# Kernel optimization log

Measured on AMD Instinct MI355X. Metric: run time of the kernel, lower is better.

The kernel has to match this reference:

```python
import jax, jax.numpy as jnp
import numpy as np

B, D, K = 8192, 256, 3
ALPHA, LAMBDA_NEG, GAMMA_SEMI = 0.7, 0.7, 0.7


def setup_inputs() -> dict:
    key = jax.random.key(0)
    k1, k2, k3 = jax.random.split(key, 3)
    text_embeddings = jax.random.normal(k1, (B, D), dtype=jnp.float32)
    image_embeddings = jax.random.normal(k2, (B, D), dtype=jnp.float32)
    # resolved pseudo-GT indices; -1 marks 'id not found in batch'
    semi_positive_indices = jax.random.randint(k3, (B, K), -1, B).astype(jnp.int32)
    return {
        "text_embeddings": text_embeddings,
        "image_embeddings": image_embeddings,
        "semi_positive_indices": semi_positive_indices,
    }


def _l2_normalize(x, eps=1e-12):
    n = jnp.sqrt(jnp.sum(x * x, axis=1, keepdims=True))
    return x / jnp.maximum(n, eps)


def reference(text_embeddings, image_embeddings, semi_positive_indices):
    t = _l2_normalize(text_embeddings)
    v = _l2_normalize(image_embeddings)
    sim = t @ v.T  # [B, B]
    b = sim.shape[0]

    rows = jnp.arange(b, dtype=semi_positive_indices.dtype)[:, None]  # [B,1]
    idx = semi_positive_indices  # [B,K]
    valid = (idx >= 0) & (idx != rows)  # exclude missing ids and the diagonal
    safe_idx = jnp.clip(idx, 0, b - 1)
    rows_b = jnp.broadcast_to(rows, idx.shape)
    semi_mask = jnp.zeros((b, b), dtype=bool).at[rows_b, safe_idx].max(valid)

    eye = jnp.eye(b, dtype=bool)
    diag = jnp.diagonal(sim)
    l_pos = jnp.sum((diag - 1.0) ** 2)

    semi_term = jnp.where(semi_mask, jnp.maximum(ALPHA - sim, 0.0), 0.0)
    l_semi_pos = jnp.sum(semi_term ** 2)

    neg_mask = ~(eye | semi_mask)
    neg_term = jnp.where(neg_mask, jnp.maximum(sim, 0.0), 0.0)
    l_neg = jnp.sum(neg_term ** 2)

    return l_pos + LAMBDA_NEG * l_neg + GAMMA_SEMI * l_semi_pos
```

## Files before the change

### kernel.cpp

```cpp
#include <hip/hip_runtime.h>

#define BDIM 8192
#define DDIM 256
#define NSLOTS 512

typedef __bf16 bf16x8 __attribute__((ext_vector_type(8)));
typedef float f32x4 __attribute__((ext_vector_type(4)));
typedef unsigned short u16x4 __attribute__((ext_vector_type(4)));

#define MEMF() asm volatile("" ::: "memory")
#define BARR()                       \
  do {                               \
    MEMF();                          \
    __builtin_amdgcn_s_barrier();    \
    MEMF();                          \
  } while (0)
#define VMW(n) asm volatile("s_waitcnt vmcnt(" #n ")" ::: "memory")

__device__ inline unsigned short f2bf(float f) {
  unsigned u = __float_as_uint(f);
  u += 0x7FFFu + ((u >> 16) & 1u);
  return (unsigned short)(u >> 16);
}
__device__ inline float bf2f(unsigned short h) {
  return __uint_as_float(((unsigned)h) << 16);
}

__device__ inline void gload_lds16(const void* g, void* l) {
  __builtin_amdgcn_global_load_lds(
      (const __attribute__((address_space(1))) void*)g,
      (__attribute__((address_space(3))) void*)l, 16, 0, 0);
}

__global__ __launch_bounds__(256) void norm_convert_kernel(
    const float* __restrict__ t, const float* __restrict__ v,
    unsigned short* __restrict__ tn, unsigned short* __restrict__ vn,
    float* __restrict__ slots) {
  int wid = threadIdx.x >> 6, lane = threadIdx.x & 63;
  if (blockIdx.x == 0) {
    slots[threadIdx.x] = 0.0f;
    slots[threadIdx.x + 256] = 0.0f;
  }
  int row = blockIdx.x * 4 + wid;
  const float* src;
  unsigned short* dst;
  if (row < BDIM) {
    src = t + (size_t)row * DDIM;
    dst = tn + (size_t)row * DDIM;
  } else {
    int r = row - BDIM;
    src = v + (size_t)r * DDIM;
    dst = vn + (size_t)r * DDIM;
  }
  float4 x = reinterpret_cast<const float4*>(src)[lane];
  float ss = x.x * x.x + x.y * x.y + x.z * x.z + x.w * x.w;
  #pragma unroll
  for (int off = 1; off < 64; off <<= 1) ss += __shfl_xor(ss, off, 64);
  float sc = 1.0f / fmaxf(sqrtf(ss), 1e-12f);
  u16x4 w;
  w[0] = f2bf(x.x * sc); w[1] = f2bf(x.y * sc);
  w[2] = f2bf(x.z * sc); w[3] = f2bf(x.w * sc);
  reinterpret_cast<u16x4*>(dst)[lane] = w;
}

__global__ __launch_bounds__(512) void loss_kernel(
    const unsigned short* __restrict__ tn,
    const unsigned short* __restrict__ vn, float* __restrict__ slots) {
  __shared__ unsigned short Asb[2][16384];
  __shared__ unsigned short Bsb[2][16384];
  __shared__ float rbuf[8];

  const int tid = threadIdx.x;
  const int lane = tid & 63;
  const int wid = tid >> 6;
  const int l15 = lane & 15;
  const int l4 = lane >> 4;
  const int wm = wid >> 2;
  const int wn = wid & 3;

  const int flat = blockIdx.x;
  const int xcd = flat & 7;
  const int s = flat >> 3;
  const int r = s >> 5;
  const int p = s & 31;
  const int rowp = (xcd >> 2) * 16 + r * 4 + (p >> 3);
  const int colp = (xcd & 3) * 8 + (p & 7);
  const int rowBase = rowp * 256;
  const int colBase = colp * 256;

  const int sg = (tid & 7) ^ ((tid >> 3) & 7);
  const unsigned short* gAsrc =
      tn + (size_t)(rowBase + (tid >> 3)) * DDIM + sg * 8;
  const unsigned short* gBsrc =
      vn + (size_t)(colBase + (tid >> 3)) * DDIM + sg * 8;
  const int ldsStage = wid * 512;

  auto stA = [&](int ob, int rg, int kt) {
    gload_lds16(gAsrc + (size_t)rg * 64 * DDIM + kt * 64,
                &Asb[ob][rg * 4096 + ldsStage]);
  };
  auto stB = [&](int ob, int rg, int kt) {
    gload_lds16(gBsrc + (size_t)rg * 64 * DDIM + kt * 64,
                &Bsb[ob][rg * 4096 + ldsStage]);
  };

  f32x4 acc[8][4];
  #pragma unroll
  for (int i = 0; i < 8; ++i)
    #pragma unroll
    for (int j = 0; j < 4; ++j) acc[i][j] = (f32x4)(0.0f);

  bf16x8 af[4][2], bv0[2][2], bv1[2][2];

  auto readA = [&](int cur, int mh) {
    #pragma unroll
    for (int mm = 0; mm < 4; ++mm) {
      const int row = wm * 128 + (mh * 4 + mm) * 16 + l15;
      #pragma unroll
      for (int kk = 0; kk < 2; ++kk) {
        const int gg = (kk * 4 + l4) ^ (l15 & 7);
        af[mm][kk] =
            *reinterpret_cast<const bf16x8*>(&Asb[cur][row * 64 + gg * 8]);
      }
    }
  };
  auto readB = [&](int cur, int nh, bf16x8 (&bv)[2][2]) {
    #pragma unroll
    for (int nn = 0; nn < 2; ++nn) {
      const int row = wn * 64 + (nh * 2 + nn) * 16 + l15;
      #pragma unroll
      for (int kk = 0; kk < 2; ++kk) {
        const int gg = (kk * 4 + l4) ^ (l15 & 7);
        bv[nn][kk] =
            *reinterpret_cast<const bf16x8*>(&Bsb[cur][row * 64 + gg * 8]);
      }
    }
  };
  auto mfmaQ = [&](int mh, int nh, bf16x8 (&bv)[2][2]) {
    __builtin_amdgcn_s_setprio(1);
    #pragma unroll
    for (int mm = 0; mm < 4; ++mm)
      #pragma unroll
      for (int nn = 0; nn < 2; ++nn)
        #pragma unroll
        for (int kk = 0; kk < 2; ++kk)
          acc[mh * 4 + mm][nh * 2 + nn] =
              __builtin_amdgcn_mfma_f32_16x16x32_bf16(
                  af[mm][kk], bv[nn][kk], acc[mh * 4 + mm][nh * 2 + nn], 0, 0,
                  0);
    __builtin_amdgcn_s_setprio(0);
  };

  stB(0, 0, 0); stB(0, 1, 0); stB(0, 2, 0); stB(0, 3, 0);
  stA(0, 0, 0); stA(0, 1, 0); stA(0, 2, 0); stA(0, 3, 0);
  VMW(0);
  BARR();

  #pragma unroll
  for (int t = 0; t < 4; ++t) {
    const int cur = t & 1, ob = cur ^ 1, kt = t + 1;
    if (t < 3) {
      stB(ob, 0, kt); stB(ob, 1, kt); stB(ob, 2, kt); stB(ob, 3, kt);
      stA(ob, 0, kt); stA(ob, 1, kt); stA(ob, 2, kt); stA(ob, 3, kt);
    }
    readA(cur, 0);
    readB(cur, 0, bv0);
    readB(cur, 1, bv1);
    mfmaQ(0, 0, bv0);
    mfmaQ(0, 1, bv1);
    readA(cur, 1);
    mfmaQ(1, 1, bv1);
    mfmaQ(1, 0, bv0);
    if (t < 3) {
      VMW(0);
      BARR();
    }
  }

  float lsum = 0.0f;
  #pragma unroll
  for (int m = 0; m < 8; ++m)
    #pragma unroll
    for (int n = 0; n < 4; ++n)
      #pragma unroll
      for (int r2 = 0; r2 < 4; ++r2) {
        float u = fmaxf(acc[m][n][r2], 0.0f);
        lsum = fmaf(u, u, lsum);
      }
  lsum *= 0.7f;
  #pragma unroll
  for (int off = 1; off < 64; off <<= 1) lsum += __shfl_xor(lsum, off, 64);
  if (lane == 0) rbuf[wid] = lsum;
  __syncthreads();
  if (tid == 0) {
    float sacc = 0.0f;
    #pragma unroll
    for (int w = 0; w < 8; ++w) sacc += rbuf[w];
    atomicAdd(&slots[flat & (NSLOTS - 1)], sacc);
  }
}

__global__ __launch_bounds__(256) void corr_kernel(
    const unsigned short* __restrict__ tn,
    const unsigned short* __restrict__ vn, const int* __restrict__ sidx,
    float* __restrict__ slots) {
  int wid = threadIdx.x >> 6, lane = threadIdx.x & 63;
  int i = blockIdx.x * 4 + wid;

  u16x4 ta = reinterpret_cast<const u16x4*>(tn + (size_t)i * DDIM)[lane];
  float t0 = bf2f(ta[0]), t1 = bf2f(ta[1]), t2 = bf2f(ta[2]), t3 = bf2f(ta[3]);

  int j0 = sidx[(size_t)i * 3 + 0];
  int j1 = sidx[(size_t)i * 3 + 1];
  int j2 = sidx[(size_t)i * 3 + 2];
  bool v0 = (j0 >= 0) & (j0 < BDIM) & (j0 != i);
  bool v1 = (j1 >= 0) & (j1 < BDIM) & (j1 != i) & !(v0 & (j1 == j0));
  bool v2 = (j2 >= 0) & (j2 < BDIM) & (j2 != i) & !(v0 & (j2 == j0)) &
            !(v1 & (j2 == j1));

  float corr = 0.0f;
  {
    u16x4 va = reinterpret_cast<const u16x4*>(vn + (size_t)i * DDIM)[lane];
    float d = t0 * bf2f(va[0]) + t1 * bf2f(va[1]) + t2 * bf2f(va[2]) +
              t3 * bf2f(va[3]);
    #pragma unroll
    for (int off = 1; off < 64; off <<= 1) d += __shfl_xor(d, off, 64);
    float u = fmaxf(d, 0.0f);
    corr += (d - 1.0f) * (d - 1.0f) - 0.7f * u * u;
  }
  int jj[3] = {j0, j1, j2};
  bool vv[3] = {v0, v1, v2};
  #pragma unroll
  for (int k = 0; k < 3; ++k) {
    int j = vv[k] ? jj[k] : i;
    u16x4 va = reinterpret_cast<const u16x4*>(vn + (size_t)j * DDIM)[lane];
    float d = t0 * bf2f(va[0]) + t1 * bf2f(va[1]) + t2 * bf2f(va[2]) +
              t3 * bf2f(va[3]);
    #pragma unroll
    for (int off = 1; off < 64; off <<= 1) d += __shfl_xor(d, off, 64);
    if (vv[k]) {
      float up = fmaxf(0.7f - d, 0.0f);
      float un = fmaxf(d, 0.0f);
      corr += 0.7f * (up * up - un * un);
    }
  }
  if (lane == 0) atomicAdd(&slots[i & (NSLOTS - 1)], corr);
}

__global__ __launch_bounds__(256) void reduce_kernel(
    const float* __restrict__ slots, float* __restrict__ out) {
  __shared__ float rb[4];
  int tid = threadIdx.x;
  float s = slots[tid] + slots[tid + 256];
  #pragma unroll
  for (int off = 1; off < 64; off <<= 1) s += __shfl_xor(s, off, 64);
  if ((tid & 63) == 0) rb[tid >> 6] = s;
  __syncthreads();
  if (tid == 0) out[0] = rb[0] + rb[1] + rb[2] + rb[3];
}

extern "C" void kernel_launch(void* const* d_in, const int* in_sizes, int n_in,
                              void* d_out, int out_size, void* d_ws,
                              size_t ws_size, hipStream_t stream) {
  const float* t = (const float*)d_in[0];
  const float* v = (const float*)d_in[1];
  const int* sidx = (const int*)d_in[2];
  float* out = (float*)d_out;
  float* slots = (float*)d_ws;
  unsigned short* tn = (unsigned short*)((char*)d_ws + 4096);
  unsigned short* vn = tn + (size_t)BDIM * DDIM;

  norm_convert_kernel<<<4096, 256, 0, stream>>>(t, v, tn, vn, slots);
  loss_kernel<<<1024, 512, 0, stream>>>(tn, vn, slots);
  corr_kernel<<<2048, 256, 0, stream>>>(tn, vn, sidx, slots);
  reduce_kernel<<<1, 256, 0, stream>>>(slots, out);
}
```

Before: 56.35 us.

## Use 4 waves per block with 128x128 per-wave tiles in loss GEMM

The loss kernel drops from 8 waves to 4 per 256x256 block tile, so each wave now computes a 128x128 sub-tile (8x8 MFMA accumulators) instead of 128x64. Each thread issues twice as many global-to-LDS loads, and the interleaved read and MFMA schedule with setprio is replaced by loading all fragments and then running the MFMAs. The aim is more register-level reuse of A and B fragments and fewer LDS reads per MFMA. The cost is much higher register pressure (256 accumulator floats per lane), less latency hiding from having fewer waves, and the loss of the previous read/compute interleaving.

```diff
diff --git a/kernel.cpp b/kernel.cpp
--- a/kernel.cpp
+++ b/kernel.cpp
@@ -63,20 +63,20 @@
   reinterpret_cast<u16x4*>(dst)[lane] = w;
 }
 
-__global__ __launch_bounds__(512) void loss_kernel(
+__global__ __launch_bounds__(256, 1) void loss_kernel(
     const unsigned short* __restrict__ tn,
     const unsigned short* __restrict__ vn, float* __restrict__ slots) {
   __shared__ unsigned short Asb[2][16384];
   __shared__ unsigned short Bsb[2][16384];
-  __shared__ float rbuf[8];
+  __shared__ float rbuf[4];
 
   const int tid = threadIdx.x;
   const int lane = tid & 63;
   const int wid = tid >> 6;
   const int l15 = lane & 15;
   const int l4 = lane >> 4;
-  const int wm = wid >> 2;
-  const int wn = wid & 3;
+  const int wm = wid >> 1;
+  const int wn = wid & 1;
 
   const int flat = blockIdx.x;
   const int xcd = flat & 7;
@@ -93,29 +93,47 @@
       tn + (size_t)(rowBase + (tid >> 3)) * DDIM + sg * 8;
   const unsigned short* gBsrc =
       vn + (size_t)(colBase + (tid >> 3)) * DDIM + sg * 8;
-  const int ldsStage = wid * 512;
+  const int ldsW = wid * 512;
 
   auto stA = [&](int ob, int rg, int kt) {
-    gload_lds16(gAsrc + (size_t)rg * 64 * DDIM + kt * 64,
-                &Asb[ob][rg * 4096 + ldsStage]);
+    #pragma unroll
+    for (int h = 0; h < 2; ++h)
+      gload_lds16(gAsrc + (size_t)(rg * 64 + h * 32) * DDIM + kt * 64,
+                  &Asb[ob][rg * 4096 + h * 2048 + ldsW]);
   };
   auto stB = [&](int ob, int rg, int kt) {
-    gload_lds16(gBsrc + (size_t)rg * 64 * DDIM + kt * 64,
-                &Bsb[ob][rg * 4096 + ldsStage]);
+    #pragma unroll
+    for (int h = 0; h < 2; ++h)
+      gload_lds16(gBsrc + (size_t)(rg * 64 + h * 32) * DDIM + kt * 64,
+                  &Bsb[ob][rg * 4096 + h * 2048 + ldsW]);
   };
 
-  f32x4 acc[8][4];
+  f32x4 acc[8][8];
   #pragma unroll
   for (int i = 0; i < 8; ++i)
     #pragma unroll
-    for (int j = 0; j < 4; ++j) acc[i][j] = (f32x4)(0.0f);
-
-  bf16x8 af[4][2], bv0[2][2], bv1[2][2];
-
-  auto readA = [&](int cur, int mh) {
-    #pragma unroll
-    for (int mm = 0; mm < 4; ++mm) {
-      const int row = wm * 128 + (mh * 4 + mm) * 16 + l15;
+    for (int j = 0; j < 8; ++j) acc[i][j] = (f32x4)(0.0f);
+
+  #pragma unroll
+  for (int rg = 0; rg < 4; ++rg) stB(0, rg, 0);
+  #pragma unroll
+  for (int rg = 0; rg < 4; ++rg) stA(0, rg, 0);
+  VMW(0);
+  BARR();
+
+  #pragma unroll
+  for (int t = 0; t < 4; ++t) {
+    const int cur = t & 1, ob = cur ^ 1, kt = t + 1;
+    if (t < 3) {
+      #pragma unroll
+      for (int rg = 0; rg < 4; ++rg) stB(ob, rg, kt);
+      #pragma unroll
+      for (int rg = 0; rg < 4; ++rg) stA(ob, rg, kt);
+    }
+    bf16x8 af[8][2], bv[8][2];
+    #pragma unroll
+    for (int mm = 0; mm < 8; ++mm) {
+      const int row = wm * 128 + mm * 16 + l15;
       #pragma unroll
       for (int kk = 0; kk < 2; ++kk) {
         const int gg = (kk * 4 + l4) ^ (l15 & 7);
@@ -123,11 +141,9 @@
             *reinterpret_cast<const bf16x8*>(&Asb[cur][row * 64 + gg * 8]);
       }
     }
-  };
-  auto readB = [&](int cur, int nh, bf16x8 (&bv)[2][2]) {
-    #pragma unroll
-    for (int nn = 0; nn < 2; ++nn) {
-      const int row = wn * 64 + (nh * 2 + nn) * 16 + l15;
+    #pragma unroll
+    for (int nn = 0; nn < 8; ++nn) {
+      const int row = wn * 128 + nn * 16 + l15;
       #pragma unroll
       for (int kk = 0; kk < 2; ++kk) {
         const int gg = (kk * 4 + l4) ^ (l15 & 7);
@@ -135,42 +151,14 @@
             *reinterpret_cast<const bf16x8*>(&Bsb[cur][row * 64 + gg * 8]);
       }
     }
-  };
-  auto mfmaQ = [&](int mh, int nh, bf16x8 (&bv)[2][2]) {
-    __builtin_amdgcn_s_setprio(1);
-    #pragma unroll
-    for (int mm = 0; mm < 4; ++mm)
-      #pragma unroll
-      for (int nn = 0; nn < 2; ++nn)
+    #pragma unroll
+    for (int kk = 0; kk < 2; ++kk)
+      #pragma unroll
+      for (int mm = 0; mm < 8; ++mm)
         #pragma unroll
-        for (int kk = 0; kk < 2; ++kk)
-          acc[mh * 4 + mm][nh * 2 + nn] =
-              __builtin_amdgcn_mfma_f32_16x16x32_bf16(
-                  af[mm][kk], bv[nn][kk], acc[mh * 4 + mm][nh * 2 + nn], 0, 0,
-                  0);
-    __builtin_amdgcn_s_setprio(0);
-  };
-
-  stB(0, 0, 0); stB(0, 1, 0); stB(0, 2, 0); stB(0, 3, 0);
-  stA(0, 0, 0); stA(0, 1, 0); stA(0, 2, 0); stA(0, 3, 0);
-  VMW(0);
-  BARR();
-
-  #pragma unroll
-  for (int t = 0; t < 4; ++t) {
-    const int cur = t & 1, ob = cur ^ 1, kt = t + 1;
-    if (t < 3) {
-      stB(ob, 0, kt); stB(ob, 1, kt); stB(ob, 2, kt); stB(ob, 3, kt);
-      stA(ob, 0, kt); stA(ob, 1, kt); stA(ob, 2, kt); stA(ob, 3, kt);
-    }
-    readA(cur, 0);
-    readB(cur, 0, bv0);
-    readB(cur, 1, bv1);
-    mfmaQ(0, 0, bv0);
-    mfmaQ(0, 1, bv1);
-    readA(cur, 1);
-    mfmaQ(1, 1, bv1);
-    mfmaQ(1, 0, bv0);
+        for (int nn = 0; nn < 8; ++nn)
+          acc[mm][nn] = __builtin_amdgcn_mfma_f32_16x16x32_bf16(
+              af[mm][kk], bv[nn][kk], acc[mm][nn], 0, 0, 0);
     if (t < 3) {
       VMW(0);
       BARR();
@@ -181,7 +169,7 @@
   #pragma unroll
   for (int m = 0; m < 8; ++m)
     #pragma unroll
-    for (int n = 0; n < 4; ++n)
+    for (int n = 0; n < 8; ++n)
       #pragma unroll
       for (int r2 = 0; r2 < 4; ++r2) {
         float u = fmaxf(acc[m][n][r2], 0.0f);
@@ -193,10 +181,8 @@
   if (lane == 0) rbuf[wid] = lsum;
   __syncthreads();
   if (tid == 0) {
-    float sacc = 0.0f;
-    #pragma unroll
-    for (int w = 0; w < 8; ++w) sacc += rbuf[w];
-    atomicAdd(&slots[flat & (NSLOTS - 1)], sacc);
+    atomicAdd(&slots[flat & (NSLOTS - 1)],
+              rbuf[0] + rbuf[1] + rbuf[2] + rbuf[3]);
   }
 }
 
@@ -271,7 +257,7 @@
   unsigned short* vn = tn + (size_t)BDIM * DDIM;
 
   norm_convert_kernel<<<4096, 256, 0, stream>>>(t, v, tn, vn, slots);
-  loss_kernel<<<1024, 512, 0, stream>>>(tn, vn, slots);
+  loss_kernel<<<1024, 256, 0, stream>>>(tn, vn, slots);
   corr_kernel<<<2048, 256, 0, stream>>>(tn, vn, sidx, slots);
   reduce_kernel<<<1, 256, 0, stream>>>(slots, out);
 }
```

New measurement: 66.70 us. 1.18x slower.

## Load A fragments directly from global memory and fold final reduction into corr kernel

Applied to the files above, without the earlier changes.

The loss GEMM no longer stages the A (text) tile through LDS. Each wave reads its A fragments straight from global memory into registers, which halves LDS usage and removes the A global-to-LDS copies. The separate reduce kernel is dropped: the last corr block, found with an atomic counter, performs the final slot reduction, saving one kernel launch. The trade-off is uncoalesced, latency-exposed global loads for A that are not prefetched ahead of the MFMAs, plus extra fences and a counter atomic.

```diff
diff --git a/kernel.cpp b/kernel.cpp
--- a/kernel.cpp
+++ b/kernel.cpp
@@ -35,11 +35,12 @@
 __global__ __launch_bounds__(256) void norm_convert_kernel(
     const float* __restrict__ t, const float* __restrict__ v,
     unsigned short* __restrict__ tn, unsigned short* __restrict__ vn,
-    float* __restrict__ slots) {
+    float* __restrict__ slots, unsigned* __restrict__ cnt) {
   int wid = threadIdx.x >> 6, lane = threadIdx.x & 63;
   if (blockIdx.x == 0) {
     slots[threadIdx.x] = 0.0f;
     slots[threadIdx.x + 256] = 0.0f;
+    if (threadIdx.x == 0) cnt[0] = 0u;
   }
   int row = blockIdx.x * 4 + wid;
   const float* src;
@@ -66,7 +67,6 @@
 __global__ __launch_bounds__(512) void loss_kernel(
     const unsigned short* __restrict__ tn,
     const unsigned short* __restrict__ vn, float* __restrict__ slots) {
-  __shared__ unsigned short Asb[2][16384];
   __shared__ unsigned short Bsb[2][16384];
   __shared__ float rbuf[8];
 
@@ -89,21 +89,18 @@
   const int colBase = colp * 256;
 
   const int sg = (tid & 7) ^ ((tid >> 3) & 7);
-  const unsigned short* gAsrc =
-      tn + (size_t)(rowBase + (tid >> 3)) * DDIM + sg * 8;
   const unsigned short* gBsrc =
       vn + (size_t)(colBase + (tid >> 3)) * DDIM + sg * 8;
   const int ldsStage = wid * 512;
 
-  auto stA = [&](int ob, int rg, int kt) {
-    gload_lds16(gAsrc + (size_t)rg * 64 * DDIM + kt * 64,
-                &Asb[ob][rg * 4096 + ldsStage]);
-  };
   auto stB = [&](int ob, int rg, int kt) {
     gload_lds16(gBsrc + (size_t)rg * 64 * DDIM + kt * 64,
                 &Bsb[ob][rg * 4096 + ldsStage]);
   };
 
+  const unsigned short* pA =
+      tn + (size_t)(rowBase + wm * 128 + l15) * DDIM + l4 * 8;
+
   f32x4 acc[8][4];
   #pragma unroll
   for (int i = 0; i < 8; ++i)
@@ -112,17 +109,13 @@
 
   bf16x8 af[4][2], bv0[2][2], bv1[2][2];
 
-  auto readA = [&](int cur, int mh) {
-    #pragma unroll
-    for (int mm = 0; mm < 4; ++mm) {
-      const int row = wm * 128 + (mh * 4 + mm) * 16 + l15;
-      #pragma unroll
-      for (int kk = 0; kk < 2; ++kk) {
-        const int gg = (kk * 4 + l4) ^ (l15 & 7);
-        af[mm][kk] =
-            *reinterpret_cast<const bf16x8*>(&Asb[cur][row * 64 + gg * 8]);
-      }
-    }
+  auto readAg = [&](int t, int mh) {
+    #pragma unroll
+    for (int mm = 0; mm < 4; ++mm)
+      #pragma unroll
+      for (int kk = 0; kk < 2; ++kk)
+        af[mm][kk] = *reinterpret_cast<const bf16x8*>(
+            pA + (size_t)(mh * 64 + mm * 16) * DDIM + t * 64 + kk * 32);
   };
   auto readB = [&](int cur, int nh, bf16x8 (&bv)[2][2]) {
     #pragma unroll
@@ -152,7 +145,6 @@
   };
 
   stB(0, 0, 0); stB(0, 1, 0); stB(0, 2, 0); stB(0, 3, 0);
-  stA(0, 0, 0); stA(0, 1, 0); stA(0, 2, 0); stA(0, 3, 0);
   VMW(0);
   BARR();
 
@@ -161,14 +153,13 @@
     const int cur = t & 1, ob = cur ^ 1, kt = t + 1;
     if (t < 3) {
       stB(ob, 0, kt); stB(ob, 1, kt); stB(ob, 2, kt); stB(ob, 3, kt);
-      stA(ob, 0, kt); stA(ob, 1, kt); stA(ob, 2, kt); stA(ob, 3, kt);
-    }
-    readA(cur, 0);
+    }
+    readAg(t, 0);
     readB(cur, 0, bv0);
     readB(cur, 1, bv1);
     mfmaQ(0, 0, bv0);
     mfmaQ(0, 1, bv1);
-    readA(cur, 1);
+    readAg(t, 1);
     mfmaQ(1, 1, bv1);
     mfmaQ(1, 0, bv0);
     if (t < 3) {
@@ -203,7 +194,10 @@
 __global__ __launch_bounds__(256) void corr_kernel(
     const unsigned short* __restrict__ tn,
     const unsigned short* __restrict__ vn, const int* __restrict__ sidx,
-    float* __restrict__ slots) {
+    float* __restrict__ slots, unsigned* __restrict__ cnt,
+    float* __restrict__ out) {
+  __shared__ int lastf;
+  __shared__ float rb[4];
   int wid = threadIdx.x >> 6, lane = threadIdx.x & 63;
   int i = blockIdx.x * 4 + wid;
 
@@ -245,18 +239,27 @@
     }
   }
   if (lane == 0) atomicAdd(&slots[i & (NSLOTS - 1)], corr);
-}
-
-__global__ __launch_bounds__(256) void reduce_kernel(
-    const float* __restrict__ slots, float* __restrict__ out) {
-  __shared__ float rb[4];
-  int tid = threadIdx.x;
-  float s = slots[tid] + slots[tid + 256];
-  #pragma unroll
-  for (int off = 1; off < 64; off <<= 1) s += __shfl_xor(s, off, 64);
-  if ((tid & 63) == 0) rb[tid >> 6] = s;
+
   __syncthreads();
-  if (tid == 0) out[0] = rb[0] + rb[1] + rb[2] + rb[3];
+  if (threadIdx.x == 0) {
+    __threadfence();
+    unsigned old = atomicAdd(cnt, 1u);
+    lastf = (old == 2047u) ? 1 : 0;
+  }
+  __syncthreads();
+  if (lastf) {
+    __threadfence();
+    int tid = threadIdx.x;
+    float sv = __hip_atomic_load(&slots[tid], __ATOMIC_RELAXED,
+                                 __HIP_MEMORY_SCOPE_AGENT) +
+               __hip_atomic_load(&slots[tid + 256], __ATOMIC_RELAXED,
+                                 __HIP_MEMORY_SCOPE_AGENT);
+    #pragma unroll
+    for (int off = 1; off < 64; off <<= 1) sv += __shfl_xor(sv, off, 64);
+    if ((tid & 63) == 0) rb[tid >> 6] = sv;
+    __syncthreads();
+    if (tid == 0) out[0] = rb[0] + rb[1] + rb[2] + rb[3];
+  }
 }
 
 extern "C" void kernel_launch(void* const* d_in, const int* in_sizes, int n_in,
@@ -267,11 +270,11 @@
   const int* sidx = (const int*)d_in[2];
   float* out = (float*)d_out;
   float* slots = (float*)d_ws;
+  unsigned* cnt = (unsigned*)((char*)d_ws + 2048);
   unsigned short* tn = (unsigned short*)((char*)d_ws + 4096);
   unsigned short* vn = tn + (size_t)BDIM * DDIM;
 
-  norm_convert_kernel<<<4096, 256, 0, stream>>>(t, v, tn, vn, slots);
+  norm_convert_kernel<<<4096, 256, 0, stream>>>(t, v, tn, vn, slots, cnt);
   loss_kernel<<<1024, 512, 0, stream>>>(tn, vn, slots);
-  corr_kernel<<<2048, 256, 0, stream>>>(tn, vn, sidx, slots);
-  reduce_kernel<<<1, 256, 0, stream>>>(slots, out);
-}
+  corr_kernel<<<2048, 256, 0, stream>>>(tn, vn, sidx, slots, cnt, out);
+}
```

Result: slower. 129.8 us (+130.4%).

## Fuse GEMM loss, correction and final reduction into one kernel

Applied to the files above, without the earlier changes.

Merges the tiled similarity-loss kernel, the per-row correction kernel and the final reduction into a single launch. The extra 128 blocks handle the correction terms, 64 rows each, alongside the GEMM tiles. The last block to finish, found with a global atomic counter, sums the 512 slots and writes the output. This removes two kernel launches and the gaps between them, and lets the correction work run alongside the GEMM tail. In exchange it adds a threadfence and atomic handshake per block, and the correction blocks now reserve the large LDS footprint of the GEMM path.

```diff
diff --git a/kernel.cpp b/kernel.cpp
--- a/kernel.cpp
+++ b/kernel.cpp
@@ -35,11 +35,12 @@
 __global__ __launch_bounds__(256) void norm_convert_kernel(
     const float* __restrict__ t, const float* __restrict__ v,
     unsigned short* __restrict__ tn, unsigned short* __restrict__ vn,
-    float* __restrict__ slots) {
+    float* __restrict__ slots, unsigned* __restrict__ cnt) {
   int wid = threadIdx.x >> 6, lane = threadIdx.x & 63;
   if (blockIdx.x == 0) {
     slots[threadIdx.x] = 0.0f;
     slots[threadIdx.x + 256] = 0.0f;
+    if (threadIdx.x == 0) cnt[0] = 0u;
   }
   int row = blockIdx.x * 4 + wid;
   const float* src;
@@ -63,200 +64,215 @@
   reinterpret_cast<u16x4*>(dst)[lane] = w;
 }
 
-__global__ __launch_bounds__(512) void loss_kernel(
+__global__ __launch_bounds__(512) void fused_kernel(
     const unsigned short* __restrict__ tn,
-    const unsigned short* __restrict__ vn, float* __restrict__ slots) {
+    const unsigned short* __restrict__ vn, const int* __restrict__ sidx,
+    float* __restrict__ slots, unsigned* __restrict__ cnt,
+    float* __restrict__ out) {
   __shared__ unsigned short Asb[2][16384];
   __shared__ unsigned short Bsb[2][16384];
   __shared__ float rbuf[8];
+  __shared__ int lastf;
 
   const int tid = threadIdx.x;
+  const int bid = blockIdx.x;
   const int lane = tid & 63;
   const int wid = tid >> 6;
-  const int l15 = lane & 15;
-  const int l4 = lane >> 4;
-  const int wm = wid >> 2;
-  const int wn = wid & 3;
-
-  const int flat = blockIdx.x;
-  const int xcd = flat & 7;
-  const int s = flat >> 3;
-  const int r = s >> 5;
-  const int p = s & 31;
-  const int rowp = (xcd >> 2) * 16 + r * 4 + (p >> 3);
-  const int colp = (xcd & 3) * 8 + (p & 7);
-  const int rowBase = rowp * 256;
-  const int colBase = colp * 256;
-
-  const int sg = (tid & 7) ^ ((tid >> 3) & 7);
-  const unsigned short* gAsrc =
-      tn + (size_t)(rowBase + (tid >> 3)) * DDIM + sg * 8;
-  const unsigned short* gBsrc =
-      vn + (size_t)(colBase + (tid >> 3)) * DDIM + sg * 8;
-  const int ldsStage = wid * 512;
-
-  auto stA = [&](int ob, int rg, int kt) {
-    gload_lds16(gAsrc + (size_t)rg * 64 * DDIM + kt * 64,
-                &Asb[ob][rg * 4096 + ldsStage]);
-  };
-  auto stB = [&](int ob, int rg, int kt) {
-    gload_lds16(gBsrc + (size_t)rg * 64 * DDIM + kt * 64,
-                &Bsb[ob][rg * 4096 + ldsStage]);
-  };
-
-  f32x4 acc[8][4];
-  #pragma unroll
-  for (int i = 0; i < 8; ++i)
-    #pragma unroll
-    for (int j = 0; j < 4; ++j) acc[i][j] = (f32x4)(0.0f);
-
-  bf16x8 af[4][2], bv0[2][2], bv1[2][2];
-
-  auto readA = [&](int cur, int mh) {
-    #pragma unroll
-    for (int mm = 0; mm < 4; ++mm) {
-      const int row = wm * 128 + (mh * 4 + mm) * 16 + l15;
-      #pragma unroll
-      for (int kk = 0; kk < 2; ++kk) {
-        const int gg = (kk * 4 + l4) ^ (l15 & 7);
-        af[mm][kk] =
-            *reinterpret_cast<const bf16x8*>(&Asb[cur][row * 64 + gg * 8]);
-      }
-    }
-  };
-  auto readB = [&](int cur, int nh, bf16x8 (&bv)[2][2]) {
-    #pragma unroll
-    for (int nn = 0; nn < 2; ++nn) {
-      const int row = wn * 64 + (nh * 2 + nn) * 16 + l15;
-      #pragma unroll
-      for (int kk = 0; kk < 2; ++kk) {
-        const int gg = (kk * 4 + l4) ^ (l15 & 7);
-        bv[nn][kk] =
-            *reinterpret_cast<const bf16x8*>(&Bsb[cur][row * 64 + gg * 8]);
-      }
-    }
-  };
-  auto mfmaQ = [&](int mh, int nh, bf16x8 (&bv)[2][2]) {
-    __builtin_amdgcn_s_setprio(1);
-    #pragma unroll
-    for (int mm = 0; mm < 4; ++mm)
-      #pragma unroll
-      for (int nn = 0; nn < 2; ++nn)
-        #pragma unroll
-        for (int kk = 0; kk < 2; ++kk)
-          acc[mh * 4 + mm][nh * 2 + nn] =
-              __builtin_amdgcn_mfma_f32_16x16x32_bf16(
-                  af[mm][kk], bv[nn][kk], acc[mh * 4 + mm][nh * 2 + nn], 0, 0,
-                  0);
-    __builtin_amdgcn_s_setprio(0);
-  };
-
-  stB(0, 0, 0); stB(0, 1, 0); stB(0, 2, 0); stB(0, 3, 0);
-  stA(0, 0, 0); stA(0, 1, 0); stA(0, 2, 0); stA(0, 3, 0);
-  VMW(0);
-  BARR();
-
-  #pragma unroll
-  for (int t = 0; t < 4; ++t) {
-    const int cur = t & 1, ob = cur ^ 1, kt = t + 1;
-    if (t < 3) {
-      stB(ob, 0, kt); stB(ob, 1, kt); stB(ob, 2, kt); stB(ob, 3, kt);
-      stA(ob, 0, kt); stA(ob, 1, kt); stA(ob, 2, kt); stA(ob, 3, kt);
-    }
-    readA(cur, 0);
-    readB(cur, 0, bv0);
-    readB(cur, 1, bv1);
-    mfmaQ(0, 0, bv0);
-    mfmaQ(0, 1, bv1);
-    readA(cur, 1);
-    mfmaQ(1, 1, bv1);
-    mfmaQ(1, 0, bv0);
-    if (t < 3) {
-      VMW(0);
-      BARR();
-    }
-  }
-
-  float lsum = 0.0f;
-  #pragma unroll
-  for (int m = 0; m < 8; ++m)
-    #pragma unroll
-    for (int n = 0; n < 4; ++n)
-      #pragma unroll
-      for (int r2 = 0; r2 < 4; ++r2) {
-        float u = fmaxf(acc[m][n][r2], 0.0f);
-        lsum = fmaf(u, u, lsum);
-      }
-  lsum *= 0.7f;
-  #pragma unroll
-  for (int off = 1; off < 64; off <<= 1) lsum += __shfl_xor(lsum, off, 64);
-  if (lane == 0) rbuf[wid] = lsum;
+
+  if (bid < 1024) {
+    const int l15 = lane & 15;
+    const int l4 = lane >> 4;
+    const int wm = wid >> 2;
+    const int wn = wid & 3;
+
+    const int xcd = bid & 7;
+    const int s = bid >> 3;
+    const int r = s >> 5;
+    const int p = s & 31;
+    const int rowp = (xcd >> 2) * 16 + r * 4 + (p >> 3);
+    const int colp = (xcd & 3) * 8 + (p & 7);
+    const int rowBase = rowp * 256;
+    const int colBase = colp * 256;
+
+    const int sg = (tid & 7) ^ ((tid >> 3) & 7);
+    const unsigned short* gAsrc =
+        tn + (size_t)(rowBase + (tid >> 3)) * DDIM + sg * 8;
+    const unsigned short* gBsrc =
+        vn + (size_t)(colBase + (tid >> 3)) * DDIM + sg * 8;
+    const int ldsStage = wid * 512;
+
+    auto stA = [&](int ob, int rg, int kt) {
+      gload_lds16(gAsrc + (size_t)rg * 64 * DDIM + kt * 64,
+                  &Asb[ob][rg * 4096 + ldsStage]);
+    };
+    auto stB = [&](int ob, int rg, int kt) {
+      gload_lds16(gBsrc + (size_t)rg * 64 * DDIM + kt * 64,
+                  &Bsb[ob][rg * 4096 + ldsStage]);
+    };
+
+    f32x4 acc[8][4];
+    #pragma unroll
+    for (int i = 0; i < 8; ++i)
+      #pragma unroll
+      for (int j = 0; j < 4; ++j) acc[i][j] = (f32x4)(0.0f);
+
+    bf16x8 af[4][2], bv0[2][2], bv1[2][2];
+
+    auto readA = [&](int cur, int mh) {
+      #pragma unroll
+      for (int mm = 0; mm < 4; ++mm) {
+        const int row = wm * 128 + (mh * 4 + mm) * 16 + l15;
+        #pragma unroll
+        for (int kk = 0; kk < 2; ++kk) {
+          const int gg = (kk * 4 + l4) ^ (l15 & 7);
+          af[mm][kk] =
+              *reinterpret_cast<const bf16x8*>(&Asb[cur][row * 64 + gg * 8]);
+        }
+      }
+    };
+    auto readB = [&](int cur, int nh, bf16x8 (&bv)[2][2]) {
+      #pragma unroll
+      for (int nn = 0; nn < 2; ++nn) {
+        const int row = wn * 64 + (nh * 2 + nn) * 16 + l15;
+        #pragma unroll
+        for (int kk = 0; kk < 2; ++kk) {
+          const int gg = (kk * 4 + l4) ^ (l15 & 7);
+          bv[nn][kk] =
+              *reinterpret_cast<const bf16x8*>(&Bsb[cur][row * 64 + gg * 8]);
+        }
+      }
+    };
+    auto mfmaQ = [&](int mh, int nh, bf16x8 (&bv)[2][2]) {
+      __builtin_amdgcn_s_setprio(1);
+      #pragma unroll
+      for (int mm = 0; mm < 4; ++mm)
+        #pragma unroll
+        for (int nn = 0; nn < 2; ++nn)
+          #pragma unroll
+          for (int kk = 0; kk < 2; ++kk)
+            acc[mh * 4 + mm][nh * 2 + nn] =
+                __builtin_amdgcn_mfma_f32_16x16x32_bf16(
+                    af[mm][kk], bv[nn][kk], acc[mh * 4 + mm][nh * 2 + nn], 0,
+                    0, 0);
+      __builtin_amdgcn_s_setprio(0);
+    };
+
+    stB(0, 0, 0); stB(0, 1, 0); stB(0, 2, 0); stB(0, 3, 0);
+    stA(0, 0, 0); stA(0, 1, 0); stA(0, 2, 0); stA(0, 3, 0);
+    VMW(0);
+    BARR();
+
+    #pragma unroll
+    for (int t = 0; t < 4; ++t) {
+      const int cur = t & 1, ob = cur ^ 1, kt = t + 1;
+      if (t < 3) {
+        stB(ob, 0, kt); stB(ob, 1, kt); stB(ob, 2, kt); stB(ob, 3, kt);
+        stA(ob, 0, kt); stA(ob, 1, kt); stA(ob, 2, kt); stA(ob, 3, kt);
+      }
+      readA(cur, 0);
+      readB(cur, 0, bv0);
+      readB(cur, 1, bv1);
+      mfmaQ(0, 0, bv0);
+      mfmaQ(0, 1, bv1);
+      readA(cur, 1);
+      mfmaQ(1, 1, bv1);
+      mfmaQ(1, 0, bv0);
+      if (t < 3) {
+        VMW(0);
+        BARR();
+      }
+    }
+
+    float lsum = 0.0f;
+    #pragma unroll
+    for (int m = 0; m < 8; ++m)
+      #pragma unroll
+      for (int n = 0; n < 4; ++n)
+        #pragma unroll
+        for (int r2 = 0; r2 < 4; ++r2) {
+          float u = fmaxf(acc[m][n][r2], 0.0f);
+          lsum = fmaf(u, u, lsum);
+        }
+    lsum *= 0.7f;
+    #pragma unroll
+    for (int off = 1; off < 64; off <<= 1) lsum += __shfl_xor(lsum, off, 64);
+    if (lane == 0) rbuf[wid] = lsum;
+    __syncthreads();
+    if (tid == 0) {
+      float sacc = 0.0f;
+      #pragma unroll
+      for (int w = 0; w < 8; ++w) sacc += rbuf[w];
+      atomicAdd(&slots[bid & (NSLOTS - 1)], sacc);
+    }
+  } else {
+    const int cb = bid - 1024;
+    float corrw = 0.0f;
+    #pragma unroll 2
+    for (int rr = 0; rr < 8; ++rr) {
+      const int i = cb * 64 + wid * 8 + rr;
+      u16x4 ta = reinterpret_cast<const u16x4*>(tn + (size_t)i * DDIM)[lane];
+      float t0 = bf2f(ta[0]), t1 = bf2f(ta[1]);
+      float t2 = bf2f(ta[2]), t3 = bf2f(ta[3]);
+
+      int j0 = sidx[(size_t)i * 3 + 0];
+      int j1 = sidx[(size_t)i * 3 + 1];
+      int j2 = sidx[(size_t)i * 3 + 2];
+      bool v0 = (j0 >= 0) & (j0 < BDIM) & (j0 != i);
+      bool v1 = (j1 >= 0) & (j1 < BDIM) & (j1 != i) & !(v0 & (j1 == j0));
+      bool v2 = (j2 >= 0) & (j2 < BDIM) & (j2 != i) & !(v0 & (j2 == j0)) &
+                !(v1 & (j2 == j1));
+
+      {
+        u16x4 va = reinterpret_cast<const u16x4*>(vn + (size_t)i * DDIM)[lane];
+        float d = t0 * bf2f(va[0]) + t1 * bf2f(va[1]) + t2 * bf2f(va[2]) +
+                  t3 * bf2f(va[3]);
+        #pragma unroll
+        for (int off = 1; off < 64; off <<= 1) d += __shfl_xor(d, off, 64);
+        float u = fmaxf(d, 0.0f);
+        corrw += (d - 1.0f) * (d - 1.0f) - 0.7f * u * u;
+      }
+      int jj[3] = {j0, j1, j2};
+      bool vv[3] = {v0, v1, v2};
+      #pragma unroll
+      for (int k = 0; k < 3; ++k) {
+        int j = vv[k] ? jj[k] : i;
+        u16x4 va = reinterpret_cast<const u16x4*>(vn + (size_t)j * DDIM)[lane];
+        float d = t0 * bf2f(va[0]) + t1 * bf2f(va[1]) + t2 * bf2f(va[2]) +
+                  t3 * bf2f(va[3]);
+        #pragma unroll
+        for (int off = 1; off < 64; off <<= 1) d += __shfl_xor(d, off, 64);
+        if (vv[k]) {
+          float up = fmaxf(0.7f - d, 0.0f);
+          float un = fmaxf(d, 0.0f);
+          corrw += 0.7f * (up * up - un * un);
+        }
+      }
+    }
+    if (lane == 0) atomicAdd(&slots[(cb * 8 + wid) & (NSLOTS - 1)], corrw);
+  }
+
   __syncthreads();
   if (tid == 0) {
-    float sacc = 0.0f;
-    #pragma unroll
-    for (int w = 0; w < 8; ++w) sacc += rbuf[w];
-    atomicAdd(&slots[flat & (NSLOTS - 1)], sacc);
-  }
-}
-
-__global__ __launch_bounds__(256) void corr_kernel(
-    const unsigned short* __restrict__ tn,
-    const unsigned short* __restrict__ vn, const int* __restrict__ sidx,
-    float* __restrict__ slots) {
-  int wid = threadIdx.x >> 6, lane = threadIdx.x & 63;
-  int i = blockIdx.x * 4 + wid;
-
-  u16x4 ta = reinterpret_cast<const u16x4*>(tn + (size_t)i * DDIM)[lane];
-  float t0 = bf2f(ta[0]), t1 = bf2f(ta[1]), t2 = bf2f(ta[2]), t3 = bf2f(ta[3]);
-
-  int j0 = sidx[(size_t)i * 3 + 0];
-  int j1 = sidx[(size_t)i * 3 + 1];
-  int j2 = sidx[(size_t)i * 3 + 2];
-  bool v0 = (j0 >= 0) & (j0 < BDIM) & (j0 != i);
-  bool v1 = (j1 >= 0) & (j1 < BDIM) & (j1 != i) & !(v0 & (j1 == j0));
-  bool v2 = (j2 >= 0) & (j2 < BDIM) & (j2 != i) & !(v0 & (j2 == j0)) &
-            !(v1 & (j2 == j1));
-
-  float corr = 0.0f;
-  {
-    u16x4 va = reinterpret_cast<const u16x4*>(vn + (size_t)i * DDIM)[lane];
-    float d = t0 * bf2f(va[0]) + t1 * bf2f(va[1]) + t2 * bf2f(va[2]) +
-              t3 * bf2f(va[3]);
-    #pragma unroll
-    for (int off = 1; off < 64; off <<= 1) d += __shfl_xor(d, off, 64);
-    float u = fmaxf(d, 0.0f);
-    corr += (d - 1.0f) * (d - 1.0f) - 0.7f * u * u;
-  }
-  int jj[3] = {j0, j1, j2};
-  bool vv[3] = {v0, v1, v2};
-  #pragma unroll
-  for (int k = 0; k < 3; ++k) {
-    int j = vv[k] ? jj[k] : i;
-    u16x4 va = reinterpret_cast<const u16x4*>(vn + (size_t)j * DDIM)[lane];
-    float d = t0 * bf2f(va[0]) + t1 * bf2f(va[1]) + t2 * bf2f(va[2]) +
-              t3 * bf2f(va[3]);
-    #pragma unroll
-    for (int off = 1; off < 64; off <<= 1) d += __shfl_xor(d, off, 64);
-    if (vv[k]) {
-      float up = fmaxf(0.7f - d, 0.0f);
-      float un = fmaxf(d, 0.0f);
-      corr += 0.7f * (up * up - un * un);
-    }
-  }
-  if (lane == 0) atomicAdd(&slots[i & (NSLOTS - 1)], corr);
-}
-
-__global__ __launch_bounds__(256) void reduce_kernel(
-    const float* __restrict__ slots, float* __restrict__ out) {
-  __shared__ float rb[4];
-  int tid = threadIdx.x;
-  float s = slots[tid] + slots[tid + 256];
-  #pragma unroll
-  for (int off = 1; off < 64; off <<= 1) s += __shfl_xor(s, off, 64);
-  if ((tid & 63) == 0) rb[tid >> 6] = s;
+    __threadfence();
+    unsigned old = atomicAdd(cnt, 1u);
+    lastf = (old == 1151u) ? 1 : 0;
+  }
   __syncthreads();
-  if (tid == 0) out[0] = rb[0] + rb[1] + rb[2] + rb[3];
+  if (lastf) {
+    __threadfence();
+    float sv = __hip_atomic_load(&slots[tid], __ATOMIC_RELAXED,
+                                 __HIP_MEMORY_SCOPE_AGENT);
+    #pragma unroll
+    for (int off = 1; off < 64; off <<= 1) sv += __shfl_xor(sv, off, 64);
+    if (lane == 0) rbuf[wid] = sv;
+    __syncthreads();
+    if (tid == 0) {
+      float tot = 0.0f;
+      #pragma unroll
+      for (int w = 0; w < 8; ++w) tot += rbuf[w];
+      out[0] = tot;
+    }
+  }
 }
 
 extern "C" void kernel_launch(void* const* d_in, const int* in_sizes, int n_in,
@@ -267,11 +283,10 @@
   const int* sidx = (const int*)d_in[2];
   float* out = (float*)d_out;
   float* slots = (float*)d_ws;
+  unsigned* cnt = (unsigned*)((char*)d_ws + 2048);
   unsigned short* tn = (unsigned short*)((char*)d_ws + 4096);
   unsigned short* vn = tn + (size_t)BDIM * DDIM;
 
-  norm_convert_kernel<<<4096, 256, 0, stream>>>(t, v, tn, vn, slots);
-  loss_kernel<<<1024, 512, 0, stream>>>(tn, vn, slots);
-  corr_kernel<<<2048, 256, 0, stream>>>(tn, vn, sidx, slots);
-  reduce_kernel<<<1, 256, 0, stream>>>(slots, out);
-}
+  norm_convert_kernel<<<4096, 256, 0, stream>>>(t, v, tn, vn, slots, cnt);
+  fused_kernel<<<1152, 512, 0, stream>>>(tn, vn, sidx, slots, cnt, out);
+}
```

Result: slower. 71.62 us (+27.1%).
